# Kernel optimization log

Hardware: AMD Instinct MI355X
Metric: run time of the kernel (lower is better)

The kernel has to match this reference:

```python
import jax, jax.numpy as jnp
import numpy as np

D_MODEL, D_K, C_DIM = 1024, 64, 64
B, S = 4, 4096


def setup_inputs() -> dict:
    key = jax.random.key(0)
    ks = jax.random.split(key, 10)
    sc = 1.0 / np.sqrt(D_MODEL)
    return {
        "X": jax.random.normal(ks[0], (B, S, D_MODEL), jnp.float32),
        "cultural_embedding": jax.random.normal(ks[1], (B, C_DIM), jnp.float32),
        "WQ": jax.random.normal(ks[2], (D_MODEL, D_K), jnp.float32) * sc,
        "bQ": jnp.zeros((D_K,), jnp.float32),
        "WK": jax.random.normal(ks[3], (D_MODEL, D_K), jnp.float32) * sc,
        "bK": jnp.zeros((D_K,), jnp.float32),
        "WV": jax.random.normal(ks[4], (D_MODEL, D_K), jnp.float32) * sc,
        "bV": jnp.zeros((D_K,), jnp.float32),
        "WC": jax.random.normal(ks[5], (C_DIM, D_K), jnp.float32) * (1.0 / np.sqrt(C_DIM)),
        "bC": jnp.zeros((D_K,), jnp.float32),
        "lam": jnp.float32(1.0),
    }


def reference(X, cultural_embedding, WQ, bQ, WK, bK, WV, bV, WC, bC, lam):
    # Projections: [B,S,d_k]
    Q = jnp.einsum('bsm,mk->bsk', X, WQ) + bQ
    K = jnp.einsum('bsm,mk->bsk', X, WK) + bK
    V = jnp.einsum('bsm,mk->bsk', X, WV) + bV
    # Cultural projection: [B,d_k]
    c_proj = cultural_embedding @ WC + bC
    # Base attention logits [B,S,S]
    base_logits = jnp.einsum('bqk,bsk->bqs', Q, K) / jnp.sqrt(jnp.float32(D_K))
    # Rank-1 cultural bias per query row, scalar lambda gate
    cultural_bias = lam * jnp.einsum('bsd,bd->bs', Q, c_proj)  # [B,S]
    combined = base_logits + cultural_bias[..., None]
    attn = jax.nn.softmax(combined, axis=-1)
    return jnp.einsum('bqs,bsk->bqk', attn, V)
```

## Files before the change

kernel.cpp:

```cpp
#include <hip/hip_runtime.h>

#define B_  4
#define S_  4096
#define DM  1024
#define DK  64
#define NSPLIT 8
#define KSPAN (S_ / NSPLIT)
#define QT  256

typedef _Float16 half8  __attribute__((ext_vector_type(8)));
typedef _Float16 half4v __attribute__((ext_vector_type(4)));
typedef float    floatx4 __attribute__((ext_vector_type(4)));

#define QSCALE 0.18033688011112042f
#define EXP2F(x) __builtin_amdgcn_exp2f(x)

__global__ __launch_bounds__(256) void wt_kernel(
    const float* __restrict__ WQ, const float* __restrict__ WK,
    const float* __restrict__ WV, _Float16* __restrict__ Wt)
{
    const int proj = blockIdx.y;
    const float* W = (proj == 0) ? WQ : (proj == 1) ? WK : WV;
    const int k0 = blockIdx.x * 64;
    const int t = threadIdx.x;
    __shared__ float T[64][68];

    #pragma unroll
    for (int p = 0; p < 4; p++) {
        int c = p * 256 + t;
        int k = c >> 4, n4 = (c & 15) * 4;
        float4 v = *(const float4*)(W + (size_t)(k0 + k) * DK + n4);
        T[k][n4 + 0] = v.x; T[k][n4 + 1] = v.y;
        T[k][n4 + 2] = v.z; T[k][n4 + 3] = v.w;
    }
    __syncthreads();

    const int n = t >> 2, kc = (t & 3) * 16;
    half8 h0, h1;
    #pragma unroll
    for (int j = 0; j < 8; j++) h0[j] = (_Float16)T[kc + j][n];
    #pragma unroll
    for (int j = 0; j < 8; j++) h1[j] = (_Float16)T[kc + 8 + j][n];
    _Float16* dst = Wt + ((size_t)proj * 64 + n) * DM + k0 + kc;
    *(half8*)(dst)     = h0;
    *(half8*)(dst + 8) = h1;
}

__global__ __launch_bounds__(256) void proj_mfma_kernel(
    const float* __restrict__ X, const _Float16* __restrict__ Wt,
    const float* __restrict__ bQ, const float* __restrict__ bK,
    const float* __restrict__ bV,
    _Float16* __restrict__ Qh, _Float16* __restrict__ Kh,
    _Float16* __restrict__ Vt)
{
    const int r0   = blockIdx.x * 64;
    const int t    = threadIdx.x;
    const int wave = t >> 6, lane = t & 63;
    const int quad = lane >> 4, l15 = lane & 15;

    __shared__ __align__(16) _Float16 Xs[64 * 72];
    __shared__ __align__(16) _Float16 Ws[3][64 * 72];

    floatx4 acc[3][4];
    #pragma unroll
    for (int p = 0; p < 3; p++)
        #pragma unroll
        for (int nt = 0; nt < 4; nt++)
            acc[p][nt] = (floatx4){0.f, 0.f, 0.f, 0.f};

    int xrow[4], xcol[4];
    #pragma unroll
    for (int p = 0; p < 4; p++) {
        int c = p * 256 + t;
        xrow[p] = c >> 4; xcol[p] = (c & 15) * 4;
    }
    int wrow[2], wcol[2];
    #pragma unroll
    for (int p = 0; p < 2; p++) {
        int c = p * 256 + t;
        wrow[p] = c >> 3; wcol[p] = (c & 7) * 8;
    }

    float4 xr[4]; half8 wr[3][2];
    #pragma unroll
    for (int p = 0; p < 4; p++)
        xr[p] = *(const float4*)(X + (size_t)(r0 + xrow[p]) * DM + xcol[p]);
    #pragma unroll
    for (int pr = 0; pr < 3; pr++)
        #pragma unroll
        for (int p = 0; p < 2; p++)
            wr[pr][p] = *(const half8*)(Wt + ((size_t)pr * 64 + wrow[p]) * DM + wcol[p]);

    for (int kt = 0; kt < DM / 64; kt++) {
        __syncthreads();
        #pragma unroll
        for (int p = 0; p < 4; p++) {
            half4v h;
            h[0] = (_Float16)xr[p].x; h[1] = (_Float16)xr[p].y;
            h[2] = (_Float16)xr[p].z; h[3] = (_Float16)xr[p].w;
            *(half4v*)&Xs[xrow[p] * 72 + xcol[p]] = h;
        }
        #pragma unroll
        for (int pr = 0; pr < 3; pr++)
            #pragma unroll
            for (int p = 0; p < 2; p++)
                *(half8*)&Ws[pr][wrow[p] * 72 + wcol[p]] = wr[pr][p];
        __syncthreads();

        if (kt + 1 < DM / 64) {
            const int kn = (kt + 1) * 64;
            #pragma unroll
            for (int p = 0; p < 4; p++)
                xr[p] = *(const float4*)(X + (size_t)(r0 + xrow[p]) * DM + kn + xcol[p]);
            #pragma unroll
            for (int pr = 0; pr < 3; pr++)
                #pragma unroll
                for (int p = 0; p < 2; p++)
                    wr[pr][p] = *(const half8*)(Wt + ((size_t)pr * 64 + wrow[p]) * DM + kn + wcol[p]);
        }

        half8 xa0 = *(half8*)&Xs[(wave * 16 + l15) * 72 + quad * 8];
        half8 xa1 = *(half8*)&Xs[(wave * 16 + l15) * 72 + 32 + quad * 8];
        #pragma unroll
        for (int pr = 0; pr < 3; pr++) {
            #pragma unroll
            for (int nt = 0; nt < 4; nt++) {
                half8 bf0 = *(half8*)&Ws[pr][(nt * 16 + l15) * 72 + quad * 8];
                half8 bf1 = *(half8*)&Ws[pr][(nt * 16 + l15) * 72 + 32 + quad * 8];
                floatx4 a = acc[pr][nt];
                a = __builtin_amdgcn_mfma_f32_16x16x32_f16(xa0, bf0, a, 0, 0, 0);
                a = __builtin_amdgcn_mfma_f32_16x16x32_f16(xa1, bf1, a, 0, 0, 0);
                acc[pr][nt] = a;
            }
        }
    }

    float bqv[4], bkv[4], bvv[4];
    #pragma unroll
    for (int nt = 0; nt < 4; nt++) {
        bqv[nt] = bQ[nt * 16 + l15];
        bkv[nt] = bK[nt * 16 + l15];
        bvv[nt] = bV[nt * 16 + l15];
    }

    const int orow = r0 + wave * 16 + quad * 4;
    const int bidx = r0 >> 12;
    const int s0   = (r0 & (S_ - 1)) + wave * 16 + quad * 4;
    #pragma unroll
    for (int nt = 0; nt < 4; nt++) {
        const int d = nt * 16 + l15;
        #pragma unroll
        for (int i = 0; i < 4; i++) {
            Qh[(size_t)(orow + i) * DK + d] =
                (_Float16)((acc[0][nt][i] + bqv[nt]) * QSCALE);
            Kh[(size_t)(orow + i) * DK + d] =
                (_Float16)(acc[1][nt][i] + bkv[nt]);
        }
        half4v hv;
        #pragma unroll
        for (int i = 0; i < 4; i++)
            hv[i] = (_Float16)(acc[2][nt][i] + bvv[nt]);
        *(half4v*)(Vt + (size_t)bidx * DK * S_ + (size_t)d * S_ + s0) = hv;
    }
}

__global__ __launch_bounds__(512, 4) void flash_mfma_kernel(
    const _Float16* __restrict__ Qh, const _Float16* __restrict__ Kh,
    const _Float16* __restrict__ Vt, _Float16* __restrict__ Oph,
    float* __restrict__ Lp)
{
    const int b     = blockIdx.y;
    const int q0    = blockIdx.x * QT;
    const int split = blockIdx.z;
    const int kbase = split * KSPAN;
    const int t     = threadIdx.x;
    const int wave  = t >> 6, lane = t & 63;
    const int quad  = lane >> 4, l15 = lane & 15;

    __shared__ __align__(16) _Float16 Ks[64 * 72];
    __shared__ __align__(16) _Float16 Vs[64 * 72];
    __shared__ __align__(16) _Float16 QsPs[QT * 72];

    const _Float16* Qb = Qh + ((size_t)b * S_ + q0) * DK;
    const _Float16* Kb = Kh + ((size_t)b * S_ + kbase) * DK;
    const _Float16* Vb = Vt + (size_t)b * DK * S_ + kbase;

    #pragma unroll
    for (int p = 0; p < 4; p++) {
        int c = p * 512 + t;
        int r = c >> 3, col = (c & 7) * 8;
        *(half8*)&QsPs[r * 72 + col] = *(const half8*)(Qb + r * 64 + col);
    }
    __syncthreads();
    half8 qf0[2], qf1[2];
    #pragma unroll
    for (int mt = 0; mt < 2; mt++) {
        const int r = wave * 32 + mt * 16 + l15;
        qf0[mt] = *(half8*)&QsPs[r * 72 + quad * 8];
        qf1[mt] = *(half8*)&QsPs[r * 72 + 32 + quad * 8];
    }
    __syncthreads();

    _Float16* Pw = &QsPs[wave * 32 * 72];

    floatx4 acc[2][4];
    float rs[2][4];
    #pragma unroll
    for (int mt = 0; mt < 2; mt++) {
        #pragma unroll
        for (int nt = 0; nt < 4; nt++) acc[mt][nt] = (floatx4){0.f,0.f,0.f,0.f};
        #pragma unroll
        for (int i = 0; i < 4; i++) rs[mt][i] = 0.f;
    }

    const int kr = t >> 3, kcol = (t & 7) * 8;
    half8 kreg = *(const half8*)(Kb + (size_t)kr * DK + kcol);
    half8 vreg = *(const half8*)(Vb + (size_t)kr * S_ + kcol);

    for (int k0 = 0; k0 < KSPAN; k0 += 64) {
        __syncthreads();
        *(half8*)&Ks[kr * 72 + kcol] = kreg;
        *(half8*)&Vs[kr * 72 + kcol] = vreg;
        __syncthreads();

        const int kn = k0 + 64;
        if (kn < KSPAN) {
            kreg = *(const half8*)(Kb + (size_t)(kn + kr) * DK + kcol);
            vreg = *(const half8*)(Vb + (size_t)kr * S_ + kn + kcol);
        }

        floatx4 sc[2][4];
        #pragma unroll
        for (int nt = 0; nt < 4; nt++) {
            half8 kf0 = *(half8*)&Ks[(nt * 16 + l15) * 72 + quad * 8];
            half8 kf1 = *(half8*)&Ks[(nt * 16 + l15) * 72 + 32 + quad * 8];
            #pragma unroll
            for (int mt = 0; mt < 2; mt++) {
                floatx4 z = (floatx4){0.f, 0.f, 0.f, 0.f};
                z = __builtin_amdgcn_mfma_f32_16x16x32_f16(qf0[mt], kf0, z, 0, 0, 0);
                z = __builtin_amdgcn_mfma_f32_16x16x32_f16(qf1[mt], kf1, z, 0, 0, 0);
                sc[mt][nt] = z;
            }
        }

        #pragma unroll
        for (int mt = 0; mt < 2; mt++)
            #pragma unroll
            for (int nt = 0; nt < 4; nt++)
                #pragma unroll
                for (int i = 0; i < 4; i++) {
                    float pe = EXP2F(sc[mt][nt][i]);
                    rs[mt][i] += pe;
                    Pw[(mt * 16 + quad * 4 + i) * 72 + nt * 16 + l15] = (_Float16)pe;
                }

        half8 pf0[2], pf1[2];
        #pragma unroll
        for (int mt = 0; mt < 2; mt++) {
            pf0[mt] = *(half8*)&Pw[(mt * 16 + l15) * 72 + quad * 8];
            pf1[mt] = *(half8*)&Pw[(mt * 16 + l15) * 72 + 32 + quad * 8];
        }

        #pragma unroll
        for (int nt = 0; nt < 4; nt++) {
            half8 vf0 = *(half8*)&Vs[(nt * 16 + l15) * 72 + quad * 8];
            half8 vf1 = *(half8*)&Vs[(nt * 16 + l15) * 72 + 32 + quad * 8];
            #pragma unroll
            for (int mt = 0; mt < 2; mt++) {
                floatx4 a = acc[mt][nt];
                a = __builtin_amdgcn_mfma_f32_16x16x32_f16(pf0[mt], vf0, a, 0, 0, 0);
                a = __builtin_amdgcn_mfma_f32_16x16x32_f16(pf1[mt], vf1, a, 0, 0, 0);
                acc[mt][nt] = a;
            }
        }
    }

    const size_t prow = (size_t)split * B_ * S_ + (size_t)b * S_ + q0;
    #pragma unroll
    for (int mt = 0; mt < 2; mt++) {
        float inv[4];
        #pragma unroll
        for (int i = 0; i < 4; i++) {
            float r = rs[mt][i];
            #pragma unroll
            for (int off = 1; off < 16; off <<= 1)
                r += __shfl_xor(r, off, 64);
            rs[mt][i] = r;
            inv[i] = 1.0f / r;
        }
        const int rbase = wave * 32 + mt * 16 + quad * 4;
        #pragma unroll
        for (int nt = 0; nt < 4; nt++)
            #pragma unroll
            for (int i = 0; i < 4; i++)
                Oph[(prow + rbase + i) * DK + nt * 16 + l15] =
                    (_Float16)(acc[mt][nt][i] * inv[i]);
        if (l15 == 0) {
            #pragma unroll
            for (int i = 0; i < 4; i++)
                Lp[prow + rbase + i] = rs[mt][i];
        }
    }
}

__global__ __launch_bounds__(256) void combine_kernel(
    const _Float16* __restrict__ Oph, const float* __restrict__ Lp,
    float* __restrict__ O)
{
    const int r  = blockIdx.x * 16 + (threadIdx.x >> 4);
    const int d4 = (threadIdx.x & 15) * 4;
    const int NR = B_ * S_;

    float lw[NSPLIT], lsum = 0.f;
    #pragma unroll
    for (int s = 0; s < NSPLIT; s++) {
        lw[s] = Lp[(size_t)s * NR + r];
        lsum += lw[s];
    }
    const float inv = 1.0f / lsum;

    float o[4] = {0.f, 0.f, 0.f, 0.f};
    #pragma unroll
    for (int s = 0; s < NSPLIT; s++) {
        half4v h = *(const half4v*)(Oph + ((size_t)s * NR + r) * DK + d4);
        const float w = lw[s];
        #pragma unroll
        for (int j = 0; j < 4; j++) o[j] += w * (float)h[j];
    }
    float4 out;
    out.x = o[0] * inv; out.y = o[1] * inv;
    out.z = o[2] * inv; out.w = o[3] * inv;
    *(float4*)(O + (size_t)r * DK + d4) = out;
}

extern "C" void kernel_launch(void* const* d_in, const int* in_sizes, int n_in,
                              void* d_out, int out_size, void* d_ws, size_t ws_size,
                              hipStream_t stream)
{
    const float* X  = (const float*)d_in[0];
    const float* WQ = (const float*)d_in[2];
    const float* bQ = (const float*)d_in[3];
    const float* WK = (const float*)d_in[4];
    const float* bK = (const float*)d_in[5];
    const float* WV = (const float*)d_in[6];
    const float* bV = (const float*)d_in[7];

    char* ws = (char*)d_ws;
    _Float16* Qh  = (_Float16*)ws;  ws += (size_t)B_ * S_ * DK * 2;
    _Float16* Kh  = (_Float16*)ws;  ws += (size_t)B_ * S_ * DK * 2;
    _Float16* Vt  = (_Float16*)ws;  ws += (size_t)B_ * S_ * DK * 2;
    _Float16* Wt  = (_Float16*)ws;  ws += (size_t)3 * 64 * DM * 2;
    _Float16* Oph = (_Float16*)ws;  ws += (size_t)NSPLIT * B_ * S_ * DK * 2;
    float* Lp     = (float*)ws;

    wt_kernel<<<dim3(DM / 64, 3), 256, 0, stream>>>(WQ, WK, WV, Wt);

    proj_mfma_kernel<<<dim3((B_ * S_) / 64), 256, 0, stream>>>(
        X, Wt, bQ, bK, bV, Qh, Kh, Vt);

    flash_mfma_kernel<<<dim3(S_ / QT, B_, NSPLIT), 512, 0, stream>>>(
        Qh, Kh, Vt, Oph, Lp);

    combine_kernel<<<dim3((B_ * S_) / 16), 256, 0, stream>>>(
        Oph, Lp, (float*)d_out);
}
```

Before: 157.3 us.

## Drop LDS staging in projection; load X and tiled weights directly into MFMA fragments

The weight transpose kernel now writes weights in a per-K-tile blocked layout, so each 64-wide K slice of all three projections is contiguous. The projection kernel no longer stages X and W through shared memory with two barriers per iteration. Each wave loads its X fragment straight from global memory and converts it to fp16 in registers, then reads weight fragments from the small L2-resident tiled buffer. This removes LDS traffic and synchronization, but every wave now re-reads the weights from global/L2 instead of sharing them through LDS.

Measured after the change: 185.0 us. 17.6% more time.

```diff
diff --git a/kernel.cpp b/kernel.cpp
--- a/kernel.cpp
+++ b/kernel.cpp
@@ -17,7 +17,7 @@
 
 __global__ __launch_bounds__(256) void wt_kernel(
     const float* __restrict__ WQ, const float* __restrict__ WK,
-    const float* __restrict__ WV, _Float16* __restrict__ Wt)
+    const float* __restrict__ WV, _Float16* __restrict__ Wt2)
 {
     const int proj = blockIdx.y;
     const float* W = (proj == 0) ? WQ : (proj == 1) ? WK : WV;
@@ -41,95 +41,68 @@
     for (int j = 0; j < 8; j++) h0[j] = (_Float16)T[kc + j][n];
     #pragma unroll
     for (int j = 0; j < 8; j++) h1[j] = (_Float16)T[kc + 8 + j][n];
-    _Float16* dst = Wt + ((size_t)proj * 64 + n) * DM + k0 + kc;
+    _Float16* dst = Wt2 + (((size_t)blockIdx.x * 3 + proj) * 64 + n) * 64 + kc;
     *(half8*)(dst)     = h0;
     *(half8*)(dst + 8) = h1;
 }
 
 __global__ __launch_bounds__(256) void proj_mfma_kernel(
-    const float* __restrict__ X, const _Float16* __restrict__ Wt,
+    const float* __restrict__ X, const _Float16* __restrict__ Wt2,
     const float* __restrict__ bQ, const float* __restrict__ bK,
     const float* __restrict__ bV,
     _Float16* __restrict__ Qh, _Float16* __restrict__ Kh,
     _Float16* __restrict__ Vt)
 {
-    const int r0   = blockIdx.x * 64;
     const int t    = threadIdx.x;
     const int wave = t >> 6, lane = t & 63;
     const int quad = lane >> 4, l15 = lane & 15;
-
-    __shared__ __align__(16) _Float16 Xs[64 * 72];
-    __shared__ __align__(16) _Float16 Ws[3][64 * 72];
+    const int row0 = blockIdx.x * 64 + wave * 16;
+
+    const float* xp = X + (size_t)(row0 + l15) * DM + quad * 8;
 
     floatx4 acc[3][4];
     #pragma unroll
-    for (int p = 0; p < 3; p++)
+    for (int pr = 0; pr < 3; pr++)
         #pragma unroll
         for (int nt = 0; nt < 4; nt++)
-            acc[p][nt] = (floatx4){0.f, 0.f, 0.f, 0.f};
-
-    int xrow[4], xcol[4];
-    #pragma unroll
-    for (int p = 0; p < 4; p++) {
-        int c = p * 256 + t;
-        xrow[p] = c >> 4; xcol[p] = (c & 15) * 4;
-    }
-    int wrow[2], wcol[2];
-    #pragma unroll
-    for (int p = 0; p < 2; p++) {
-        int c = p * 256 + t;
-        wrow[p] = c >> 3; wcol[p] = (c & 7) * 8;
-    }
-
-    float4 xr[4]; half8 wr[3][2];
-    #pragma unroll
-    for (int p = 0; p < 4; p++)
-        xr[p] = *(const float4*)(X + (size_t)(r0 + xrow[p]) * DM + xcol[p]);
-    #pragma unroll
-    for (int pr = 0; pr < 3; pr++)
-        #pragma unroll
-        for (int p = 0; p < 2; p++)
-            wr[pr][p] = *(const half8*)(Wt + ((size_t)pr * 64 + wrow[p]) * DM + wcol[p]);
+            acc[pr][nt] = (floatx4){0.f, 0.f, 0.f, 0.f};
+
+    float4 xa = *(const float4*)(xp + 0);
+    float4 xb = *(const float4*)(xp + 4);
+    float4 xc = *(const float4*)(xp + 32);
+    float4 xd = *(const float4*)(xp + 36);
 
     for (int kt = 0; kt < DM / 64; kt++) {
-        __syncthreads();
-        #pragma unroll
-        for (int p = 0; p < 4; p++) {
-            half4v h;
-            h[0] = (_Float16)xr[p].x; h[1] = (_Float16)xr[p].y;
-            h[2] = (_Float16)xr[p].z; h[3] = (_Float16)xr[p].w;
-            *(half4v*)&Xs[xrow[p] * 72 + xcol[p]] = h;
-        }
-        #pragma unroll
-        for (int pr = 0; pr < 3; pr++)
-            #pragma unroll
-            for (int p = 0; p < 2; p++)
-                *(half8*)&Ws[pr][wrow[p] * 72 + wcol[p]] = wr[pr][p];
-        __syncthreads();
+        half8 xf0, xf1;
+        xf0[0] = (_Float16)xa.x; xf0[1] = (_Float16)xa.y;
+        xf0[2] = (_Float16)xa.z; xf0[3] = (_Float16)xa.w;
+        xf0[4] = (_Float16)xb.x; xf0[5] = (_Float16)xb.y;
+        xf0[6] = (_Float16)xb.z; xf0[7] = (_Float16)xb.w;
+        xf1[0] = (_Float16)xc.x; xf1[1] = (_Float16)xc.y;
+        xf1[2] = (_Float16)xc.z; xf1[3] = (_Float16)xc.w;
+        xf1[4] = (_Float16)xd.x; xf1[5] = (_Float16)xd.y;
+        xf1[6] = (_Float16)xd.z; xf1[7] = (_Float16)xd.w;
 
         if (kt + 1 < DM / 64) {
             const int kn = (kt + 1) * 64;
-            #pragma unroll
-            for (int p = 0; p < 4; p++)
-                xr[p] = *(const float4*)(X + (size_t)(r0 + xrow[p]) * DM + kn + xcol[p]);
-            #pragma unroll
-            for (int pr = 0; pr < 3; pr++)
-                #pragma unroll
-                for (int p = 0; p < 2; p++)
-                    wr[pr][p] = *(const half8*)(Wt + ((size_t)pr * 64 + wrow[p]) * DM + kn + wcol[p]);
-        }
-
-        half8 xa0 = *(half8*)&Xs[(wave * 16 + l15) * 72 + quad * 8];
-        half8 xa1 = *(half8*)&Xs[(wave * 16 + l15) * 72 + 32 + quad * 8];
+            xa = *(const float4*)(xp + kn + 0);
+            xb = *(const float4*)(xp + kn + 4);
+            xc = *(const float4*)(xp + kn + 32);
+            xd = *(const float4*)(xp + kn + 36);
+        }
+
+        const _Float16* wb =
+            Wt2 + ((size_t)kt * 3 * 64) * 64 + (size_t)l15 * 64 + quad * 8;
         #pragma unroll
         for (int pr = 0; pr < 3; pr++) {
             #pragma unroll
             for (int nt = 0; nt < 4; nt++) {
-                half8 bf0 = *(half8*)&Ws[pr][(nt * 16 + l15) * 72 + quad * 8];
-                half8 bf1 = *(half8*)&Ws[pr][(nt * 16 + l15) * 72 + 32 + quad * 8];
+                const _Float16* wp = wb + (size_t)(pr * 64 + nt * 16) * 64;
+                half8 w0 = *(const half8*)(wp);
+                half8 w1 = *(const half8*)(wp + 32);
                 floatx4 a = acc[pr][nt];
-                a = __builtin_amdgcn_mfma_f32_16x16x32_f16(xa0, bf0, a, 0, 0, 0);
-                a = __builtin_amdgcn_mfma_f32_16x16x32_f16(xa1, bf1, a, 0, 0, 0);
+                a = __builtin_amdgcn_mfma_f32_16x16x32_f16(xf0, w0, a, 0, 0, 0);
+                a = __builtin_amdgcn_mfma_f32_16x16x32_f16(xf1, w1, a, 0, 0, 0);
                 acc[pr][nt] = a;
             }
         }
@@ -143,9 +116,9 @@
         bvv[nt] = bV[nt * 16 + l15];
     }
 
-    const int orow = r0 + wave * 16 + quad * 4;
-    const int bidx = r0 >> 12;
-    const int s0   = (r0 & (S_ - 1)) + wave * 16 + quad * 4;
+    const int orow = row0 + quad * 4;
+    const int bidx = row0 >> 12;
+    const int s0   = (row0 & (S_ - 1)) + quad * 4;
     #pragma unroll
     for (int nt = 0; nt < 4; nt++) {
         const int d = nt * 16 + l15;
@@ -349,14 +322,14 @@
     _Float16* Qh  = (_Float16*)ws;  ws += (size_t)B_ * S_ * DK * 2;
     _Float16* Kh  = (_Float16*)ws;  ws += (size_t)B_ * S_ * DK * 2;
     _Float16* Vt  = (_Float16*)ws;  ws += (size_t)B_ * S_ * DK * 2;
-    _Float16* Wt  = (_Float16*)ws;  ws += (size_t)3 * 64 * DM * 2;
+    _Float16* Wt2 = (_Float16*)ws;  ws += (size_t)3 * 64 * DM * 2;
     _Float16* Oph = (_Float16*)ws;  ws += (size_t)NSPLIT * B_ * S_ * DK * 2;
     float* Lp     = (float*)ws;
 
-    wt_kernel<<<dim3(DM / 64, 3), 256, 0, stream>>>(WQ, WK, WV, Wt);
+    wt_kernel<<<dim3(DM / 64, 3), 256, 0, stream>>>(WQ, WK, WV, Wt2);
 
     proj_mfma_kernel<<<dim3((B_ * S_) / 64), 256, 0, stream>>>(
-        X, Wt, bQ, bK, bV, Qh, Kh, Vt);
+        X, Wt2, bQ, bK, bV, Qh, Kh, Vt);
 
     flash_mfma_kernel<<<dim3(S_ / QT, B_, NSPLIT), 512, 0, stream>>>(
         Qh, Kh, Vt, Oph, Lp);
```
